# Optimization experiments

Hardware: AMD Instinct MI355X
Metric: run time of the kernel (lower is better)

## Reference

```python
import jax, jax.numpy as jnp
import numpy as np

N = 100000      # num nodes
E = 1600000     # num edges (avg degree 16)
D_IN = 128
D_OUT = 128
EPS = 1e-12     # F.normalize default eps


def setup_inputs() -> dict:
    key = jax.random.key(0)
    k1, k2, k3, k4 = jax.random.split(key, 4)
    x = jax.random.normal(k1, (N, D_IN), dtype=jnp.float32)
    row = jax.random.randint(k2, (E,), 0, N, dtype=jnp.int32)
    # guarantee no self loops in the raw graph: col = (row + offset) % N, offset in [1, N)
    offset = jax.random.randint(k3, (E,), 1, N, dtype=jnp.int32)
    col = (row + offset) % N
    edge_index = jnp.stack([row, col], axis=0)
    # xavier_uniform_ for weight [in, out]
    a = np.sqrt(6.0 / (D_IN + D_OUT)).astype(np.float32)
    weight = jax.random.uniform(k4, (D_IN, D_OUT), dtype=jnp.float32, minval=-a, maxval=a)
    return {"x": x, "edge_index": edge_index, "weight": weight}


def reference(x, edge_index, weight):
    row, col = edge_index[0], edge_index[1]
    # remove_self_loops: drop edges with row == col (mask keeps shapes static)
    mask = (row != col)
    # linear transform first (as in the original forward)
    xw = jnp.matmul(x, weight)                               # [N, D_OUT]
    # scatter_mean over edges with self loops added:
    # out[i] = (sum_{j->i, j!=i} xw[j] + xw[i]) / (deg_nonself(i) + 1)
    msg = jnp.where(mask[:, None], xw[col], jnp.float32(0.0))  # [E, D_OUT]
    seg_sum = jax.ops.segment_sum(msg, row, num_segments=N) + xw
    cnt = jax.ops.segment_sum(mask.astype(xw.dtype), row, num_segments=N) + jnp.float32(1.0)
    out = seg_sum / cnt[:, None]
    # F.normalize(out, p=2, dim=-1): out / max(||out||_2, eps)
    norm = jnp.sqrt(jnp.sum(out * out, axis=-1, keepdims=True))
    out = out / jnp.maximum(norm, jnp.float32(EPS))
    return out
```

## Files before the change

### kernel.cpp

```cpp
#include <hip/hip_runtime.h>
#include <hip/hip_fp16.h>
#include <stdint.h>

#define NN 100000
#define NE 1600000
#define DD 128

#define NBKT 391
#define CAPB 4480
#define NBIN 3125
#define GCAP 1024

typedef _Float16 f16x8 __attribute__((ext_vector_type(8)));
typedef float f32x4 __attribute__((ext_vector_type(4)));

__device__ __forceinline__ uint32_t hadd2u(uint32_t a, uint32_t b){
  union { uint32_t u; __half2 h; } x, y;
  x.u = a; y.u = b;
  x.h = __hadd2(x.h, y.h);
  return x.u;
}
__device__ __forceinline__ uint32_t hmul2u(uint32_t a, __half2 m){
  union { uint32_t u; __half2 h; } x; x.u = a;
  x.h = __hmul2(x.h, m);
  return x.u;
}

__global__ __launch_bounds__(256) void k_part1(
    const int* __restrict__ ei, int* __restrict__ bktres, uint32_t* __restrict__ ibuf,
    const float* __restrict__ w, uint16_t* __restrict__ wsw){
  int b = blockIdx.x, t = threadIdx.x;
  if (b < NBKT){
    __shared__ int sh[NBKT];
    int e0 = b*4096;
    for (int i=t; i<NBKT; i+=256) sh[i] = 0;
    __syncthreads();
    int rr[16], cc[16];
    #pragma unroll
    for (int j=0;j<16;j++){
      int e = e0 + j*256 + t;
      rr[j] = -1;
      if (e < NE){
        rr[j] = ei[e]; cc[j] = ei[NE + e];
        atomicAdd(&sh[rr[j] >> 8], 1);
      }
    }
    __syncthreads();
    for (int i=t; i<NBKT; i+=256){
      int v = sh[i];
      sh[i] = v ? atomicAdd(&bktres[i*16], v) : 0;
    }
    __syncthreads();
    #pragma unroll
    for (int j=0;j<16;j++){
      if (rr[j] >= 0){
        int bk = rr[j] >> 8;
        int p = atomicAdd(&sh[bk], 1);
        if (p < CAPB)
          ibuf[(size_t)bk*CAPB + p] = (uint32_t)(((rr[j] & 255) << 17) | cc[j]);
      }
    }
  } else {
    int wi = (b - NBKT)*256 + t;
    int j = wi & 7, l = (wi >> 3) & 63, kt = (wi >> 9) & 3, ct = wi >> 11;
    int k = kt*32 + ((l >> 4) & 3)*8 + j;
    int d = ct*16 + (l & 15);
    union { _Float16 h; uint16_t u; } cv; cv.h = (_Float16)w[k*DD + d];
    wsw[wi] = cv.u;
  }
}

__global__ __launch_bounds__(256) void k_mid(
    const int* __restrict__ bktres, uint32_t* __restrict__ ibuf,
    uint32_t* __restrict__ rowinfo,
    const float4* __restrict__ x, uint2* __restrict__ x16){
  int t = threadIdx.x, b = blockIdx.x;
  if (b >= NBKT){
    int i = (b - NBKT)*256 + t;
    float4 v = x[i];
    union { _Float16 h[4]; uint2 u; } r;
    r.h[0] = (_Float16)v.x; r.h[1] = (_Float16)v.y;
    r.h[2] = (_Float16)v.z; r.h[3] = (_Float16)v.w;
    x16[i] = r.u;
    return;
  }
  __shared__ uint32_t s_rec[CAPB];
  __shared__ int s_deg[256], s_off[256], s_cur[256];
  int lane = t & 63, wid = t >> 6;
  int cnt = bktres[b*16]; if (cnt > CAPB) cnt = CAPB;
  size_t bb = (size_t)b*CAPB;
  s_deg[t] = 0;
  __syncthreads();
  for (int i=t; i<cnt; i+=256){
    uint32_t rec = ibuf[bb + i];
    s_rec[i] = rec;
    atomicAdd(&s_deg[rec >> 17], 1);
  }
  __syncthreads();
  if (wid == 0){
    int carry = 0;
    for (int ch=0; ch<4; ch++){
      int idx = ch*64 + lane;
      int o = s_deg[idx], v = o;
      #pragma unroll
      for (int d=1; d<64; d<<=1){ int y = __shfl_up(v, d); if (lane >= d) v += y; }
      int ex = carry + v - o;
      s_off[idx] = ex; s_cur[idx] = ex;
      carry += __shfl(v, 63);
    }
  }
  __syncthreads();
  int dgc = s_deg[t] > 255 ? 255 : s_deg[t];
  rowinfo[b*256 + t] = ((uint32_t)s_off[t] << 8) | (uint32_t)dgc;
  for (int i=t; i<cnt; i+=256){
    uint32_t rec = s_rec[i];
    int p = atomicAdd(&s_cur[rec >> 17], 1);
    ibuf[bb + p] = rec & 0x1FFFFu;
  }
}

__global__ __launch_bounds__(256) void k_gather(
    const uint2* __restrict__ xp, const uint32_t* __restrict__ ibuf,
    const uint32_t* __restrict__ rowinfo, uint32_t* __restrict__ agg32){
  __shared__ int s_col[GCAP];
  __shared__ int s_loc[32], s_deg[32];
  int t = threadIdx.x, wid = t >> 6, lane = t & 63;
  int b = blockIdx.x;
  int row0 = b << 5;
  if (t < 32){
    uint32_t info = rowinfo[row0 + t];
    s_loc[t] = (int)(info >> 8);
    s_deg[t] = (int)(info & 255u);
  }
  __syncthreads();
  int base = s_loc[0];
  int len = s_loc[31] + s_deg[31] - base; if (len > GCAP) len = GCAP;
  size_t bb = (size_t)(row0 >> 8)*CAPB + base;
  for (int i=t; i<len; i+=256) s_col[i] = (int)ibuf[bb + i];
  __syncthreads();

  int q = lane & 31, half = lane >> 5;
  for (int lr = wid; lr < 32; lr += 4){
    int n = row0 + lr;
    int dg  = s_deg[lr];
    int off = s_loc[lr] - base;
    uint2 sv = xp[(size_t)n*32 + q];
    uint32_t a01 = 0u, a23 = 0u;
    int j = 0;
    for (; j+16 <= dg; j += 16){
      int c0 = s_col[off+j+half],    c1 = s_col[off+j+2+half];
      int c2 = s_col[off+j+4+half],  c3 = s_col[off+j+6+half];
      int c4 = s_col[off+j+8+half],  c5 = s_col[off+j+10+half];
      int c6 = s_col[off+j+12+half], c7 = s_col[off+j+14+half];
      uint2 v0 = xp[(size_t)c0*32 + q]; uint2 v1 = xp[(size_t)c1*32 + q];
      uint2 v2 = xp[(size_t)c2*32 + q]; uint2 v3 = xp[(size_t)c3*32 + q];
      uint2 v4 = xp[(size_t)c4*32 + q]; uint2 v5 = xp[(size_t)c5*32 + q];
      uint2 v6 = xp[(size_t)c6*32 + q]; uint2 v7 = xp[(size_t)c7*32 + q];
      a01 = hadd2u(a01, v0.x); a23 = hadd2u(a23, v0.y);
      a01 = hadd2u(a01, v1.x); a23 = hadd2u(a23, v1.y);
      a01 = hadd2u(a01, v2.x); a23 = hadd2u(a23, v2.y);
      a01 = hadd2u(a01, v3.x); a23 = hadd2u(a23, v3.y);
      a01 = hadd2u(a01, v4.x); a23 = hadd2u(a23, v4.y);
      a01 = hadd2u(a01, v5.x); a23 = hadd2u(a23, v5.y);
      a01 = hadd2u(a01, v6.x); a23 = hadd2u(a23, v6.y);
      a01 = hadd2u(a01, v7.x); a23 = hadd2u(a23, v7.y);
    }
    for (; j+8 <= dg; j += 8){
      int c0 = s_col[off+j+half],   c1 = s_col[off+j+2+half];
      int c2 = s_col[off+j+4+half], c3 = s_col[off+j+6+half];
      uint2 v0 = xp[(size_t)c0*32 + q]; uint2 v1 = xp[(size_t)c1*32 + q];
      uint2 v2 = xp[(size_t)c2*32 + q]; uint2 v3 = xp[(size_t)c3*32 + q];
      a01 = hadd2u(a01, v0.x); a23 = hadd2u(a23, v0.y);
      a01 = hadd2u(a01, v1.x); a23 = hadd2u(a23, v1.y);
      a01 = hadd2u(a01, v2.x); a23 = hadd2u(a23, v2.y);
      a01 = hadd2u(a01, v3.x); a23 = hadd2u(a23, v3.y);
    }
    for (; j+2 <= dg; j += 2){
      int c0 = s_col[off+j+half];
      uint2 v0 = xp[(size_t)c0*32 + q];
      a01 = hadd2u(a01, v0.x); a23 = hadd2u(a23, v0.y);
    }
    if (j < dg){
      int c0 = s_col[off+j];
      uint2 v0 = xp[(size_t)c0*32 + q];
      a01 = hadd2u(a01, half ? 0u : v0.x);
      a23 = hadd2u(a23, half ? 0u : v0.y);
    }
    a01 = hadd2u(a01, (uint32_t)__shfl_xor((int)a01, 32));
    a23 = hadd2u(a23, (uint32_t)__shfl_xor((int)a23, 32));
    __half2 inv2 = __float2half2_rn(1.0f / (float)(dg + 1));
    uint32_t r01 = hmul2u(hadd2u(a01, sv.x), inv2);
    uint32_t r23 = hmul2u(hadd2u(a23, sv.y), inv2);
    agg32[(size_t)n*64 + (q << 1) + half] = half ? r23 : r01;
  }
}

__global__ __launch_bounds__(256) void k_gemm(const uint16_t* __restrict__ agg,
                                              const uint16_t* __restrict__ wsw,
                                              float* __restrict__ out){
  int tid = threadIdx.x, wid = tid >> 6, lane = tid & 63;
  int g = blockIdx.x*4 + wid;
  if (g >= 6250) return;
  const char* aggb = (const char*)agg;
  const f16x8* Bf = (const f16x8*)wsw;
  int row = g*16 + (lane & 15), gk = lane >> 4;
  f16x8 a[4];
  #pragma unroll
  for (int kt=0; kt<4; kt++)
    a[kt] = *(const f16x8*)(aggb + (size_t)row*256 + kt*64 + gk*16);

  f32x4 acc[8];
  #pragma unroll
  for (int ct=0;ct<8;ct++) acc[ct] = (f32x4){0.f,0.f,0.f,0.f};
  #pragma unroll
  for (int ct=0;ct<8;ct++){
    #pragma unroll
    for (int kt=0;kt<4;kt++)
      acc[ct] = __builtin_amdgcn_mfma_f32_16x16x32_f16(a[kt], Bf[(ct*4+kt)*64 + lane], acc[ct], 0, 0, 0);
  }
  float sq[4] = {0.f,0.f,0.f,0.f};
  #pragma unroll
  for (int ct=0;ct<8;ct++){
    #pragma unroll
    for (int i=0;i<4;i++) sq[i] += acc[ct][i]*acc[ct][i];
  }
  #pragma unroll
  for (int m=1;m<16;m<<=1){
    #pragma unroll
    for (int i=0;i<4;i++) sq[i] += __shfl_xor(sq[i], m);
  }
  float sc4[4];
  #pragma unroll
  for (int i=0;i<4;i++) sc4[i] = 1.0f / fmaxf(sqrtf(sq[i]), 1e-12f);

  int col = lane & 15;
  int rb = g*16 + (gk << 2);
  #pragma unroll
  for (int i=0;i<4;i++){
    int n = rb + i;
    #pragma unroll
    for (int ct=0;ct<8;ct++)
      out[(size_t)n*DD + (ct<<4) + col] = acc[ct][i]*sc4[i];
  }
}

extern "C" void kernel_launch(void* const* d_in, const int* in_sizes, int n_in,
                              void* d_out, int out_size, void* d_ws, size_t ws_size,
                              hipStream_t stream){
  const float* x = (const float*)d_in[0];
  const int*  ei = (const int*)d_in[1];
  const float* w = (const float*)d_in[2];
  float* out = (float*)d_out;
  char* ws = (char*)d_ws;
  (void)in_sizes; (void)n_in; (void)out_size; (void)ws_size;

  size_t off = 0;
  uint16_t* x16 = (uint16_t*)(ws + off); off += (size_t)NN*DD*2;
  uint16_t* agg = (uint16_t*)(ws + off); off += (size_t)NN*DD*2;
  uint16_t* wsw = (uint16_t*)(ws + off); off += (size_t)DD*DD*2;
  uint32_t* ibuf = (uint32_t*)(ws + off); off += (size_t)NBKT*CAPB*4;
  int* bktres   = (int*)(ws + off); off += (size_t)NBKT*16*4;
  uint32_t* rowinfo = (uint32_t*)(ws + off); off += (size_t)NBKT*256*4;

  hipMemsetAsync(bktres, 0, (size_t)NBKT*16*4, stream);
  k_part1<<<NBKT + 64, 256, 0, stream>>>(ei, bktres, ibuf, w, wsw);
  k_mid<<<NBKT + 12500, 256, 0, stream>>>(bktres, ibuf, rowinfo, (const float4*)x, (uint2*)x16);
  k_gather<<<NBIN, 256, 0, stream>>>((const uint2*)x16, ibuf, rowinfo, (uint32_t*)agg);
  k_gemm<<<1563, 256, 0, stream>>>(agg, wsw, out);
}
```

Baseline: 134.0 us.

## Split fp16 features into 8 column slices for cache-local gather

Stores the fp16 node features as 8 slices of 16 columns, one contiguous 3.2MB array per slice. The gather launches 8x as many blocks, and each block aggregates one slice for 32 rows with 8 lanes per row. The aim is for each slice's working set to fit in L2/MALL so random neighbour reads hit cache. The cost is that column indices are reloaded 8 times, and lanes in a wavefront now loop to the maximum degree of the 8 rows they share. The GEMM reads the sliced aggregate layout.

```diff
diff --git a/kernel.cpp b/kernel.cpp
--- a/kernel.cpp
+++ b/kernel.cpp
@@ -73,7 +73,7 @@
 __global__ __launch_bounds__(256) void k_mid(
     const int* __restrict__ bktres, uint32_t* __restrict__ ibuf,
     uint32_t* __restrict__ rowinfo,
-    const float4* __restrict__ x, uint2* __restrict__ x16){
+    const float4* __restrict__ x, uint32_t* __restrict__ xs){
   int t = threadIdx.x, b = blockIdx.x;
   if (b >= NBKT){
     int i = (b - NBKT)*256 + t;
@@ -81,7 +81,9 @@
     union { _Float16 h[4]; uint2 u; } r;
     r.h[0] = (_Float16)v.x; r.h[1] = (_Float16)v.y;
     r.h[2] = (_Float16)v.z; r.h[3] = (_Float16)v.w;
-    x16[i] = r.u;
+    int n = i >> 5, dq = i & 31;
+    uint32_t* dst = xs + (size_t)(dq >> 2)*NN*8 + (size_t)n*8 + (dq & 3)*2;
+    *(uint2*)dst = r.u;
     return;
   }
   __shared__ uint32_t s_rec[CAPB];
@@ -120,13 +122,14 @@
 }
 
 __global__ __launch_bounds__(256) void k_gather(
-    const uint2* __restrict__ xp, const uint32_t* __restrict__ ibuf,
-    const uint32_t* __restrict__ rowinfo, uint32_t* __restrict__ agg32){
+    const uint32_t* __restrict__ xs, const uint32_t* __restrict__ ibuf,
+    const uint32_t* __restrict__ rowinfo, uint32_t* __restrict__ aggS){
   __shared__ int s_col[GCAP];
   __shared__ int s_loc[32], s_deg[32];
   int t = threadIdx.x, wid = t >> 6, lane = t & 63;
   int b = blockIdx.x;
-  int row0 = b << 5;
+  int bin = b >> 3, slice = b & 7;
+  int row0 = bin << 5;
   if (t < 32){
     uint32_t info = rowinfo[row0 + t];
     s_loc[t] = (int)(info >> 8);
@@ -139,60 +142,40 @@
   for (int i=t; i<len; i+=256) s_col[i] = (int)ibuf[bb + i];
   __syncthreads();
 
-  int q = lane & 31, half = lane >> 5;
-  for (int lr = wid; lr < 32; lr += 4){
-    int n = row0 + lr;
-    int dg  = s_deg[lr];
-    int off = s_loc[lr] - base;
-    uint2 sv = xp[(size_t)n*32 + q];
-    uint32_t a01 = 0u, a23 = 0u;
-    int j = 0;
-    for (; j+16 <= dg; j += 16){
-      int c0 = s_col[off+j+half],    c1 = s_col[off+j+2+half];
-      int c2 = s_col[off+j+4+half],  c3 = s_col[off+j+6+half];
-      int c4 = s_col[off+j+8+half],  c5 = s_col[off+j+10+half];
-      int c6 = s_col[off+j+12+half], c7 = s_col[off+j+14+half];
-      uint2 v0 = xp[(size_t)c0*32 + q]; uint2 v1 = xp[(size_t)c1*32 + q];
-      uint2 v2 = xp[(size_t)c2*32 + q]; uint2 v3 = xp[(size_t)c3*32 + q];
-      uint2 v4 = xp[(size_t)c4*32 + q]; uint2 v5 = xp[(size_t)c5*32 + q];
-      uint2 v6 = xp[(size_t)c6*32 + q]; uint2 v7 = xp[(size_t)c7*32 + q];
-      a01 = hadd2u(a01, v0.x); a23 = hadd2u(a23, v0.y);
-      a01 = hadd2u(a01, v1.x); a23 = hadd2u(a23, v1.y);
-      a01 = hadd2u(a01, v2.x); a23 = hadd2u(a23, v2.y);
-      a01 = hadd2u(a01, v3.x); a23 = hadd2u(a23, v3.y);
-      a01 = hadd2u(a01, v4.x); a23 = hadd2u(a23, v4.y);
-      a01 = hadd2u(a01, v5.x); a23 = hadd2u(a23, v5.y);
-      a01 = hadd2u(a01, v6.x); a23 = hadd2u(a23, v6.y);
-      a01 = hadd2u(a01, v7.x); a23 = hadd2u(a23, v7.y);
-    }
-    for (; j+8 <= dg; j += 8){
-      int c0 = s_col[off+j+half],   c1 = s_col[off+j+2+half];
-      int c2 = s_col[off+j+4+half], c3 = s_col[off+j+6+half];
-      uint2 v0 = xp[(size_t)c0*32 + q]; uint2 v1 = xp[(size_t)c1*32 + q];
-      uint2 v2 = xp[(size_t)c2*32 + q]; uint2 v3 = xp[(size_t)c3*32 + q];
-      a01 = hadd2u(a01, v0.x); a23 = hadd2u(a23, v0.y);
-      a01 = hadd2u(a01, v1.x); a23 = hadd2u(a23, v1.y);
-      a01 = hadd2u(a01, v2.x); a23 = hadd2u(a23, v2.y);
-      a01 = hadd2u(a01, v3.x); a23 = hadd2u(a23, v3.y);
-    }
-    for (; j+2 <= dg; j += 2){
-      int c0 = s_col[off+j+half];
-      uint2 v0 = xp[(size_t)c0*32 + q];
-      a01 = hadd2u(a01, v0.x); a23 = hadd2u(a23, v0.y);
-    }
-    if (j < dg){
-      int c0 = s_col[off+j];
-      uint2 v0 = xp[(size_t)c0*32 + q];
-      a01 = hadd2u(a01, half ? 0u : v0.x);
-      a23 = hadd2u(a23, half ? 0u : v0.y);
-    }
-    a01 = hadd2u(a01, (uint32_t)__shfl_xor((int)a01, 32));
-    a23 = hadd2u(a23, (uint32_t)__shfl_xor((int)a23, 32));
-    __half2 inv2 = __float2half2_rn(1.0f / (float)(dg + 1));
-    uint32_t r01 = hmul2u(hadd2u(a01, sv.x), inv2);
-    uint32_t r23 = hmul2u(hadd2u(a23, sv.y), inv2);
-    agg32[(size_t)n*64 + (q << 1) + half] = half ? r23 : r01;
-  }
+  int j = lane >> 3, w = lane & 7;
+  int lr = wid*8 + j;
+  int r = row0 + lr;
+  int dg = s_deg[lr], off = s_loc[lr] - base;
+  const uint32_t* xsl = xs + (size_t)slice*NN*8;
+  uint32_t acc = 0u;
+  int md = dg;
+  md = max(md, __shfl_xor(md, 8));
+  md = max(md, __shfl_xor(md, 16));
+  md = max(md, __shfl_xor(md, 32));
+  int s = 0;
+  for (; s+4 <= md; s += 4){
+    int i0 = off + ((s+0 < dg) ? s+0 : 0);
+    int i1 = off + ((s+1 < dg) ? s+1 : 0);
+    int i2 = off + ((s+2 < dg) ? s+2 : 0);
+    int i3 = off + ((s+3 < dg) ? s+3 : 0);
+    int c0 = s_col[i0], c1 = s_col[i1], c2 = s_col[i2], c3 = s_col[i3];
+    uint32_t v0 = xsl[(size_t)c0*8 + w];
+    uint32_t v1 = xsl[(size_t)c1*8 + w];
+    uint32_t v2 = xsl[(size_t)c2*8 + w];
+    uint32_t v3 = xsl[(size_t)c3*8 + w];
+    if (s+0 < dg) acc = hadd2u(acc, v0);
+    if (s+1 < dg) acc = hadd2u(acc, v1);
+    if (s+2 < dg) acc = hadd2u(acc, v2);
+    if (s+3 < dg) acc = hadd2u(acc, v3);
+  }
+  for (; s < md; s++){
+    int i0 = off + ((s < dg) ? s : 0);
+    uint32_t v0 = xsl[(size_t)s_col[i0]*8 + w];
+    if (s < dg) acc = hadd2u(acc, v0);
+  }
+  acc = hadd2u(acc, xsl[(size_t)r*8 + w]);
+  acc = hmul2u(acc, __float2half2_rn(1.0f / (float)(dg + 1)));
+  aggS[(size_t)slice*NN*8 + (size_t)r*8 + w] = acc;
 }
 
 __global__ __launch_bounds__(256) void k_gemm(const uint16_t* __restrict__ agg,
@@ -206,8 +189,11 @@
   int row = g*16 + (lane & 15), gk = lane >> 4;
   f16x8 a[4];
   #pragma unroll
-  for (int kt=0; kt<4; kt++)
-    a[kt] = *(const f16x8*)(aggb + (size_t)row*256 + kt*64 + gk*16);
+  for (int kt=0; kt<4; kt++){
+    int d0 = kt*32 + gk*8;
+    int slice = d0 >> 4;
+    a[kt] = *(const f16x8*)(aggb + (size_t)slice*NN*32 + (size_t)row*32 + ((d0 >> 3) & 1)*16);
+  }
 
   f32x4 acc[8];
   #pragma unroll
@@ -255,7 +241,7 @@
   (void)in_sizes; (void)n_in; (void)out_size; (void)ws_size;
 
   size_t off = 0;
-  uint16_t* x16 = (uint16_t*)(ws + off); off += (size_t)NN*DD*2;
+  uint32_t* xs  = (uint32_t*)(ws + off); off += (size_t)NN*DD*2;
   uint16_t* agg = (uint16_t*)(ws + off); off += (size_t)NN*DD*2;
   uint16_t* wsw = (uint16_t*)(ws + off); off += (size_t)DD*DD*2;
   uint32_t* ibuf = (uint32_t*)(ws + off); off += (size_t)NBKT*CAPB*4;
@@ -264,7 +250,7 @@
 
   hipMemsetAsync(bktres, 0, (size_t)NBKT*16*4, stream);
   k_part1<<<NBKT + 64, 256, 0, stream>>>(ei, bktres, ibuf, w, wsw);
-  k_mid<<<NBKT + 12500, 256, 0, stream>>>(bktres, ibuf, rowinfo, (const float4*)x, (uint2*)x16);
-  k_gather<<<NBIN, 256, 0, stream>>>((const uint2*)x16, ibuf, rowinfo, (uint32_t*)agg);
+  k_mid<<<NBKT + 12500, 256, 0, stream>>>(bktres, ibuf, rowinfo, (const float4*)x, xs);
+  k_gather<<<NBIN*8, 256, 0, stream>>>(xs, ibuf, rowinfo, (uint32_t*)agg);
   k_gemm<<<1563, 256, 0, stream>>>(agg, wsw, out);
 }
```

Result: slower. 146.0 us (+8.9%).
